# Kernel optimization log

Hardware: AMD Instinct MI355X
Metric: run time of the kernel (lower is better)

## Reference

```python
import jax, jax.numpy as jnp
import numpy as np

N_NODES = 50000
N_EDGES = 800000
IN_DIM = 128
HIDDEN = 64      # out_channels per head (concat=False -> head mean)
HEADS = 2
N_GRAPHS = 64
LN_EPS = 1e-5


def _layer_norm(x, g, b):
    mu = jnp.mean(x, axis=-1, keepdims=True)
    var = jnp.mean((x - mu) ** 2, axis=-1, keepdims=True)
    return (x - mu) * jax.lax.rsqrt(var + LN_EPS) * g + b


def _transformer_conv(x, src, dst, Wq, bq, Wk, bk, Wv, bv, Ws, bs):
    # PyG TransformerConv, concat=False, root_weight=True, beta=False.
    n = x.shape[0]
    q = (x @ Wq + bq).reshape(n, HEADS, -1)[dst]   # [E, H, D] query at target i
    k = (x @ Wk + bk).reshape(n, HEADS, -1)[src]   # [E, H, D] key at source j
    v = (x @ Wv + bv).reshape(n, HEADS, -1)[src]   # [E, H, D] value at source j
    d = q.shape[-1]
    score = jnp.sum(q * k, axis=-1) / jnp.sqrt(jnp.asarray(d, x.dtype))  # [E, H]
    # segment softmax over incoming edges of each target node
    smax = jax.ops.segment_max(score, dst, num_segments=n)
    e = jnp.exp(score - smax[dst])
    denom = jax.ops.segment_sum(e, dst, num_segments=n)
    alpha = e / denom[dst]                                              # [E, H]
    agg = jax.ops.segment_sum(alpha[..., None] * v, dst, num_segments=n)  # [N, H, D]
    out = jnp.mean(agg, axis=1)                     # concat=False -> head mean
    return out + x @ Ws + bs                        # root/skip connection


def setup_inputs() -> dict:
    key = jax.random.key(0)
    ks = jax.random.split(key, 40)
    inp = {}
    inp["x"] = jax.random.normal(ks[0], (N_NODES, IN_DIM), jnp.float32)
    inp["edge_index"] = jax.random.randint(ks[1], (2, N_EDGES), 0, N_NODES, dtype=jnp.int64)
    inp["batch"] = jnp.sort(jax.random.randint(ks[2], (N_NODES,), 0, N_GRAPHS, dtype=jnp.int64))
    dims = [(IN_DIM, HIDDEN), (HIDDEN, HIDDEN), (HIDDEN, HIDDEN)]
    i = 3
    for l, (din, dout) in enumerate(dims):
        for nm in ("q", "k", "v"):
            inp[f"W{nm}{l}"] = jax.random.normal(ks[i], (din, HEADS * dout), jnp.float32) * 0.05; i += 1
            inp[f"b{nm}{l}"] = jnp.zeros((HEADS * dout,), jnp.float32)
        inp[f"Ws{l}"] = jax.random.normal(ks[i], (din, dout), jnp.float32) * 0.05; i += 1
        inp[f"bs{l}"] = jnp.zeros((dout,), jnp.float32)
    for l in range(2):  # LayerNorm after layers 0 and 1 only
        inp[f"g{l}"] = jnp.ones((HIDDEN,), jnp.float32)
        inp[f"beta{l}"] = jnp.zeros((HIDDEN,), jnp.float32)
    inp["Wp"] = jax.random.normal(ks[i], (HIDDEN, 1), jnp.float32) * 0.05
    inp["bp"] = jnp.zeros((1,), jnp.float32)
    return inp


def reference(x, edge_index, batch,
              Wq0, bq0, Wk0, bk0, Wv0, bv0, Ws0, bs0,
              Wq1, bq1, Wk1, bk1, Wv1, bv1, Ws1, bs1,
              Wq2, bq2, Wk2, bk2, Wv2, bv2, Ws2, bs2,
              g0, beta0, g1, beta1, Wp, bp):
    src, dst = edge_index[0], edge_index[1]
    layers = [(Wq0, bq0, Wk0, bk0, Wv0, bv0, Ws0, bs0),
              (Wq1, bq1, Wk1, bk1, Wv1, bv1, Ws1, bs1),
              (Wq2, bq2, Wk2, bk2, Wv2, bv2, Ws2, bs2)]
    lns = [(g0, beta0), (g1, beta1)]
    h = x
    for i, p in enumerate(layers):
        h = _transformer_conv(h, src, dst, *p)
        h = jax.nn.relu(h)  # dropout p=0.0 / eval -> identity
        if i != len(layers) - 1:
            h = _layer_norm(h, *lns[i])
    # global mean pool per graph
    cnt = jax.ops.segment_sum(jnp.ones((h.shape[0],), h.dtype), batch, num_segments=N_GRAPHS)
    pooled = jax.ops.segment_sum(h, batch, num_segments=N_GRAPHS) / jnp.maximum(cnt, 1.0)[:, None]
    return pooled @ Wp + bp
```

## Files before the change

kernel.cpp:

```cpp
#include <hip/hip_runtime.h>
#include <hip/hip_fp16.h>
#include <math.h>

#define HIDDEN 64
#define HEADS 2
#define NCOLS 448
#define KV_COLS 256
#define KV_ROW_BYTES 512
#define N_GRAPHS 64
#define LN_EPS 1e-5f
#define Q_SCALE 0.18033688011112042f

typedef _Float16 half8 __attribute__((ext_vector_type(8)));
typedef float    f32x4 __attribute__((ext_vector_type(4)));


__global__ void cast_f2h_kernel(const float* __restrict__ in, _Float16* __restrict__ out, int n4)
{
    int i = blockIdx.x * 256 + threadIdx.x;
    if (i < n4) {
        float4 v = *(const float4*)&in[i * 4];
        __half2 a = __floats2half2_rn(v.x, v.y);
        __half2 b = __floats2half2_rn(v.z, v.w);
        uint2 pk;
        pk.x = *(unsigned int*)&a;
        pk.y = *(unsigned int*)&b;
        *(uint2*)&out[i * 4] = pk;
    }
}

__global__ void pack_kernel(const float* __restrict__ Wq, const float* __restrict__ Wk,
                            const float* __restrict__ Wv, const float* __restrict__ Ws,
                            const float* __restrict__ bq, const float* __restrict__ bk,
                            const float* __restrict__ bv, const float* __restrict__ bs,
                            _Float16* __restrict__ Bt, float* __restrict__ bcat, int K)
{
    int idx = blockIdx.x * 256 + threadIdx.x;
    int total = NCOLS * K;
    if (idx < total) {
        int c = idx / K, k = idx - c * K;
        float v;
        if      (c < 128) v = Wq[k * 128 + c] * Q_SCALE;
        else if (c < 256) v = Wk[k * 128 + (c - 128)];
        else if (c < 384) v = Wv[k * 128 + (c - 256)];
        else              v = Ws[k * 64  + (c - 384)];
        Bt[idx] = (_Float16)v;
    }
    if (idx < NCOLS) {
        float b;
        if      (idx < 128) b = bq[idx] * Q_SCALE;
        else if (idx < 256) b = bk[idx - 128];
        else if (idx < 384) b = bv[idx - 256];
        else                b = bs[idx - 384];
        bcat[idx] = b;
    }
}

template<int K, int NT>
__device__ __forceinline__ void gemm_body(
    const _Float16* __restrict__ Ah, const float* __restrict__ bias,
    _Float16* __restrict__ qh, float* __restrict__ qsk, __half* __restrict__ kvh,
    const _Float16* Bs, int M, int colBase, int chunkRow0, int tid)
{
    int lane = tid & 63;
    int w    = tid >> 6;
    int fr   = lane & 15;
    int g    = lane >> 4;
    int row0 = chunkRow0 + w * 16;
    int arow = row0 + fr;
    if (arow > M - 1) arow = M - 1;

    f32x4 acc[NT];
    #pragma unroll
    for (int c = 0; c < NT; ++c) acc[c] = (f32x4){0.f, 0.f, 0.f, 0.f};

    #pragma unroll
    for (int ks = 0; ks < K / 32; ++ks) {
        int k0 = ks * 32 + g * 8;
        half8 af = *(const half8*)&Ah[(size_t)arow * K + k0];
        #pragma unroll
        for (int c = 0; c < NT; ++c) {
            int rl   = c * 16 + fr;
            int byte = rl * (K * 2) + k0 * 2;
            int sw   = byte ^ ((rl & 7) << 4);
            half8 bf = *(const half8*)((const char*)Bs + sw);
            acc[c] = __builtin_amdgcn_mfma_f32_16x16x32_f16(af, bf, acc[c], 0, 0, 0);
        }
    }

    #pragma unroll
    for (int c = 0; c < NT; ++c) {
        int col = colBase + c * 16 + fr;
        float bs = bias[col];
        #pragma unroll
        for (int j = 0; j < 4; ++j) {
            int row = row0 + g * 4 + j;
            if (row >= M) continue;
            float o = acc[c][j] + bs;
            if (col < 128) {
                qh[(size_t)row * 128 + col] = (_Float16)o;
            } else if (col >= 384) {
                qsk[(size_t)row * 64 + (col - 384)] = o;
            } else {
                int cc  = col - 128;
                int mat = cc >> 7;
                int hh  = (cc >> 6) & 1;
                int d   = cc & 63;
                int pos = mat * 128 + (d >> 2) * 8 + hh * 4 + (d & 3);
                kvh[(size_t)row * KV_COLS + pos] = __float2half_rn(o);
            }
        }
    }
}

template<int K>
__global__ __launch_bounds__(512, 4) void gemm_mfma_kernel(
    const _Float16* __restrict__ Ah,
    const _Float16* __restrict__ Bt,
    const float* __restrict__ bias,
    _Float16* __restrict__ qh, float* __restrict__ qsk,
    __half* __restrict__ kvh, int M)
{
    __shared__ _Float16 Bs[256 * K];

    int tid    = threadIdx.x;
    int colblk = blockIdx.x & 1;
    int chunk  = blockIdx.x >> 1;
    int colBase = colblk ? 256 : 0;
    int cols    = colblk ? 192 : 256;

    int bytes = cols * K * 2;
    const char* src = (const char*)Bt + (size_t)colBase * K * 2;
    for (int i = tid * 16; i < bytes; i += 512 * 16) {
        int rl = i / (K * 2);
        int sw = i ^ ((rl & 7) << 4);
        *(half8*)((char*)Bs + sw) = *(const half8*)(src + i);
    }
    __syncthreads();

    if (colblk == 0)
        gemm_body<K, 16>(Ah, bias, qh, qsk, kvh, Bs, M, 0,   chunk * 128, tid);
    else
        gemm_body<K, 12>(Ah, bias, qh, qsk, kvh, Bs, M, 256, chunk * 128, tid);
}

__global__ void hist_kernel(const int* __restrict__ dst, int* __restrict__ counts, int E)
{
    int i = blockIdx.x * 256 + threadIdx.x;
    if (i < E) atomicAdd(&counts[dst[i]], 1);
}

__global__ __launch_bounds__(256) void block_reduce_kernel(
    const int* __restrict__ counts, int* __restrict__ bsum, int N)
{
    __shared__ int s[256];
    int t = threadIdx.x;
    int i = blockIdx.x * 256 + t;
    s[t] = (i < N) ? counts[i] : 0;
    __syncthreads();
    #pragma unroll
    for (int o = 128; o; o >>= 1) {
        if (t < o) s[t] += s[t + o];
        __syncthreads();
    }
    if (t == 0) bsum[blockIdx.x] = s[0];
}

__global__ __launch_bounds__(256) void scan_partials_kernel(
    const int* __restrict__ bsum, int* __restrict__ boff, int nb, int* __restrict__ rowN)
{
    __shared__ int s[256];
    int t = threadIdx.x;
    int v = (t < nb) ? bsum[t] : 0;
    s[t] = v;
    __syncthreads();
    #pragma unroll
    for (int o = 1; o < 256; o <<= 1) {
        int x = (t >= o) ? s[t - o] : 0;
        __syncthreads();
        s[t] += x;
        __syncthreads();
    }
    if (t < nb) boff[t] = s[t] - v;
    if (t == nb - 1) rowN[0] = s[t];
}

__global__ __launch_bounds__(256) void block_scan_kernel(
    const int* __restrict__ counts, const int* __restrict__ boff,
    int* __restrict__ row_ptr, int* __restrict__ cursor, int N)
{
    __shared__ int s[256];
    int t = threadIdx.x;
    int i = blockIdx.x * 256 + t;
    int v = (i < N) ? counts[i] : 0;
    s[t] = v;
    __syncthreads();
    #pragma unroll
    for (int o = 1; o < 256; o <<= 1) {
        int x = (t >= o) ? s[t - o] : 0;
        __syncthreads();
        s[t] += x;
        __syncthreads();
    }
    if (i < N) {
        int excl = s[t] - v + boff[blockIdx.x];
        row_ptr[i] = excl;
        cursor[i]  = excl;
    }
}

__global__ void scatter_kernel(const int* __restrict__ ei, int* __restrict__ cursor,
                               int* __restrict__ src_off, int E)
{
    int i = blockIdx.x * 256 + threadIdx.x;
    if (i < E) {
        int d = ei[E + i];
        int pos = atomicAdd(&cursor[d], 1);
        src_off[pos] = ei[i] * KV_ROW_BYTES;
    }
}

__device__ __forceinline__ float dpp_sum16(float x)
{
    float t;
    t = __int_as_float(__builtin_amdgcn_mov_dpp(__float_as_int(x), 0xB1,  0xF, 0xF, true)); x += t;
    t = __int_as_float(__builtin_amdgcn_mov_dpp(__float_as_int(x), 0x4E,  0xF, 0xF, true)); x += t;
    t = __int_as_float(__builtin_amdgcn_mov_dpp(__float_as_int(x), 0x141, 0xF, 0xF, true)); x += t;
    t = __int_as_float(__builtin_amdgcn_mov_dpp(__float_as_int(x), 0x140, 0xF, 0xF, true)); x += t;
    return x;
}

__device__ __forceinline__ void edge_step(
    const uint4& kraw, const uint4& vraw,
    const float4& q0, const float4& q1,
    float& m0, float& s0, float4& a0,
    float& m1, float& s1, float4& a1)
{
    const __half2* kp = (const __half2*)&kraw;
    float2 ka = __half22float2(kp[0]), kb = __half22float2(kp[1]);
    float2 kc = __half22float2(kp[2]), kd = __half22float2(kp[3]);

    float p0 = fmaf(q0.w, kb.y, fmaf(q0.z, kb.x, fmaf(q0.y, ka.y, q0.x * ka.x)));
    float p1 = fmaf(q1.w, kd.y, fmaf(q1.z, kd.x, fmaf(q1.y, kc.y, q1.x * kc.x)));
    float sc0 = dpp_sum16(p0);
    float sc1 = dpp_sum16(p1);

    const __half2* vp = (const __half2*)&vraw;
    float2 va = __half22float2(vp[0]), vb = __half22float2(vp[1]);
    float2 vc = __half22float2(vp[2]), vd = __half22float2(vp[3]);

    float nm0 = fmaxf(m0, sc0);
    float f0  = exp2f(m0 - nm0);
    float w0  = exp2f(sc0 - nm0);
    s0 = fmaf(s0, f0, w0);
    a0.x = fmaf(a0.x, f0, w0 * va.x);
    a0.y = fmaf(a0.y, f0, w0 * va.y);
    a0.z = fmaf(a0.z, f0, w0 * vb.x);
    a0.w = fmaf(a0.w, f0, w0 * vb.y);
    m0 = nm0;

    float nm1 = fmaxf(m1, sc1);
    float f1  = exp2f(m1 - nm1);
    float w1  = exp2f(sc1 - nm1);
    s1 = fmaf(s1, f1, w1);
    a1.x = fmaf(a1.x, f1, w1 * vc.x);
    a1.y = fmaf(a1.y, f1, w1 * vc.y);
    a1.z = fmaf(a1.z, f1, w1 * vd.x);
    a1.w = fmaf(a1.w, f1, w1 * vd.y);
    m1 = nm1;
}

__global__ __launch_bounds__(256) void edge_conv_kernel(
    const _Float16* __restrict__ qh, const float* __restrict__ qsk,
    const __half* __restrict__ kvh,
    const int* __restrict__ row_ptr, const int* __restrict__ src_off,
    const float* __restrict__ gamma, const float* __restrict__ beta,
    float* __restrict__ hout, _Float16* __restrict__ hh, int N, int do_ln)
{
    int wave = threadIdx.x >> 6;
    int lane = threadIdx.x & 63;
    int g    = lane >> 4;
    int sub  = lane & 15;
    int node = blockIdx.x * 4 + wave;
    if (node >= N) return;

    const __half* qrow = (const __half*)(qh + (size_t)node * 128);
    float4 q0, q1;
    {
        uint2 p0 = *(const uint2*)&qrow[sub * 4];
        uint2 p1 = *(const uint2*)&qrow[64 + sub * 4];
        const __half2* h0 = (const __half2*)&p0;
        const __half2* h1 = (const __half2*)&p1;
        float2 a = __half22float2(h0[0]), b = __half22float2(h0[1]);
        float2 c = __half22float2(h1[0]), d = __half22float2(h1[1]);
        q0 = make_float4(a.x, a.y, b.x, b.y);
        q1 = make_float4(c.x, c.y, d.x, d.y);
    }

    int e0 = row_ptr[node], e1 = row_ptr[node + 1];
    int deg = e1 - e0;

    float  m0 = -1e30f, m1 = -1e30f;
    float  s0 = 0.f, s1 = 0.f;
    float4 a0 = make_float4(0.f, 0.f, 0.f, 0.f);
    float4 a1 = make_float4(0.f, 0.f, 0.f, 0.f);

    const char* kvb = (const char*)kvh;
    int  e    = e0 + g;
    bool have = (e < e1);
    uint4 kA, vA, kB, vB;
    if (have) {
        const char* jb = kvb + (size_t)(unsigned)src_off[e];
        kA = *(const uint4*)(jb + sub * 16);
        vA = *(const uint4*)(jb + 256 + sub * 16);
    }

    while (have) {
        int  eB    = e + 4;
        bool haveB = (eB < e1);
        if (haveB) {
            const char* jb = kvb + (size_t)(unsigned)src_off[eB];
            kB = *(const uint4*)(jb + sub * 16);
            vB = *(const uint4*)(jb + 256 + sub * 16);
        }
        edge_step(kA, vA, q0, q1, m0, s0, a0, m1, s1, a1);
        if (!haveB) break;

        int  eA    = eB + 4;
        bool haveA = (eA < e1);
        if (haveA) {
            const char* jb = kvb + (size_t)(unsigned)src_off[eA];
            kA = *(const uint4*)(jb + sub * 16);
            vA = *(const uint4*)(jb + 256 + sub * 16);
        }
        edge_step(kB, vB, q0, q1, m0, s0, a0, m1, s1, a1);

        e = eA; have = haveA;
    }

    #pragma unroll
    for (int offm = 16; offm <= 32; offm <<= 1) {
        float mo0 = __shfl_xor(m0, offm);
        float so0 = __shfl_xor(s0, offm);
        float4 ao0;
        ao0.x = __shfl_xor(a0.x, offm); ao0.y = __shfl_xor(a0.y, offm);
        ao0.z = __shfl_xor(a0.z, offm); ao0.w = __shfl_xor(a0.w, offm);
        float nm = fmaxf(m0, mo0);
        float fa = exp2f(m0 - nm), fb = exp2f(mo0 - nm);
        s0 = s0 * fa + so0 * fb;
        a0.x = a0.x * fa + ao0.x * fb; a0.y = a0.y * fa + ao0.y * fb;
        a0.z = a0.z * fa + ao0.z * fb; a0.w = a0.w * fa + ao0.w * fb;
        m0 = nm;

        float mo1 = __shfl_xor(m1, offm);
        float so1 = __shfl_xor(s1, offm);
        float4 ao1;
        ao1.x = __shfl_xor(a1.x, offm); ao1.y = __shfl_xor(a1.y, offm);
        ao1.z = __shfl_xor(a1.z, offm); ao1.w = __shfl_xor(a1.w, offm);
        nm = fmaxf(m1, mo1);
        fa = exp2f(m1 - nm); fb = exp2f(mo1 - nm);
        s1 = s1 * fa + so1 * fb;
        a1.x = a1.x * fa + ao1.x * fb; a1.y = a1.y * fa + ao1.y * fb;
        a1.z = a1.z * fa + ao1.z * fb; a1.w = a1.w * fa + ao1.w * fb;
        m1 = nm;
    }

    float4 skip = *(const float4*)&qsk[(size_t)node * 64 + sub * 4];
    float4 o;
    if (deg > 0) {
        float r0 = 0.5f / s0, r1 = 0.5f / s1;
        o.x = a0.x * r0 + a1.x * r1 + skip.x;
        o.y = a0.y * r0 + a1.y * r1 + skip.y;
        o.z = a0.z * r0 + a1.z * r1 + skip.z;
        o.w = a0.w * r0 + a1.w * r1 + skip.w;
    } else {
        o = skip;
    }
    o.x = fmaxf(o.x, 0.f); o.y = fmaxf(o.y, 0.f);
    o.z = fmaxf(o.z, 0.f); o.w = fmaxf(o.w, 0.f);

    if (do_ln) {
        float mu = dpp_sum16(o.x + o.y + o.z + o.w) * (1.0f / 64.0f);
        float dx = o.x - mu, dy = o.y - mu, dz = o.z - mu, dw = o.w - mu;
        float var = dpp_sum16(dx * dx + dy * dy + dz * dz + dw * dw) * (1.0f / 64.0f);
        float rs = rsqrtf(var + LN_EPS);
        float4 gm = *(const float4*)&gamma[sub * 4];
        float4 bt = *(const float4*)&beta[sub * 4];
        o.x = dx * rs * gm.x + bt.x;
        o.y = dy * rs * gm.y + bt.y;
        o.z = dz * rs * gm.z + bt.z;
        o.w = dw * rs * gm.w + bt.w;
    }
    if (g == 0) {
        *(float4*)&hout[(size_t)node * HIDDEN + sub * 4] = o;
        __half2 h01 = __floats2half2_rn(o.x, o.y);
        __half2 h23 = __floats2half2_rn(o.z, o.w);
        uint2 pk;
        pk.x = *(unsigned int*)&h01;
        pk.y = *(unsigned int*)&h23;
        *(uint2*)&hh[(size_t)node * HIDDEN + sub * 4] = pk;
    }
}

#define POOL_CHUNK 32
__global__ __launch_bounds__(64) void pool_kernel(const float* __restrict__ h,
                                                  const int* __restrict__ batch,
                                                  float* __restrict__ pooled,
                                                  float* __restrict__ cnt, int N)
{
    int lane = threadIdx.x;
    int start = blockIdx.x * POOL_CHUNK;
    if (start >= N) return;
    int end = min(start + POOL_CHUNK, N);
    int b0 = batch[start];
    int b1 = batch[end - 1];

    if (b0 == b1) {
        float acc = 0.f;
        #pragma unroll 4
        for (int i = start; i < end; ++i)
            acc += h[(size_t)i * HIDDEN + lane];
        atomicAdd(&pooled[b0 * HIDDEN + lane], acc);
        if (lane == 0) atomicAdd(&cnt[b0], (float)(end - start));
    } else {
        float acc = 0.f;
        int cur = b0, c = 0;
        for (int i = start; i < end; ++i) {
            int b = batch[i];
            if (b != cur) {
                atomicAdd(&pooled[cur * HIDDEN + lane], acc);
                if (lane == 0) atomicAdd(&cnt[cur], (float)c);
                acc = 0.f; c = 0; cur = b;
            }
            acc += h[(size_t)i * HIDDEN + lane];
            ++c;
        }
        atomicAdd(&pooled[cur * HIDDEN + lane], acc);
        if (lane == 0) atomicAdd(&cnt[cur], (float)c);
    }
}

__global__ void final_kernel(const float* __restrict__ pooled, const float* __restrict__ cnt,
                             const float* __restrict__ Wp, const float* __restrict__ bp,
                             float* __restrict__ out)
{
    int g = threadIdx.x;
    float c = fmaxf(cnt[g], 1.0f);
    float s = 0.f;
    for (int d = 0; d < HIDDEN; ++d) s += pooled[g * HIDDEN + d] * Wp[d];
    out[g] = s / c + bp[0];
}

extern "C" void kernel_launch(void* const* d_in, const int* in_sizes, int n_in,
                              void* d_out, int out_size, void* d_ws, size_t ws_size,
                              hipStream_t stream)
{
    const float* x    = (const float*)d_in[0];
    const int*   ei   = (const int*)d_in[1];
    const int*   batch= (const int*)d_in[2];

    const float* Wl[3][4];
    const float* bl[3][4];
    for (int l = 0; l < 3; ++l) {
        int b = 3 + l * 8;
        Wl[l][0] = (const float*)d_in[b + 0]; bl[l][0] = (const float*)d_in[b + 1];
        Wl[l][1] = (const float*)d_in[b + 2]; bl[l][1] = (const float*)d_in[b + 3];
        Wl[l][2] = (const float*)d_in[b + 4]; bl[l][2] = (const float*)d_in[b + 5];
        Wl[l][3] = (const float*)d_in[b + 6]; bl[l][3] = (const float*)d_in[b + 7];
    }
    const float* g0    = (const float*)d_in[27];
    const float* beta0 = (const float*)d_in[28];
    const float* g1    = (const float*)d_in[29];
    const float* beta1 = (const float*)d_in[30];
    const float* Wp    = (const float*)d_in[31];
    const float* bp    = (const float*)d_in[32];

    const int N = in_sizes[0] / 128;
    const int E = in_sizes[1] / 2;

    size_t off = 0;
    auto carve = [&](size_t bytes) -> char* {
        char* p = (char*)d_ws + off;
        off = (off + bytes + 255) & ~(size_t)255;
        return p;
    };
    _Float16*  qh     = (_Float16*)carve((size_t)N * 128 * 2);
    float*     qsk    = (float*)carve((size_t)N * 64 * 4);
    __half*    kvh    = (__half*)carve((size_t)N * KV_COLS * 2);
    float*     h      = (float*)carve((size_t)N * HIDDEN * 4);
    _Float16*  hh     = (_Float16*)carve((size_t)N * HIDDEN * 2);
    _Float16*  xh     = (_Float16*)carve((size_t)N * 128 * 2);
    _Float16*  Bt     = (_Float16*)carve((size_t)NCOLS * 128 * 2);
    float*     bcat   = (float*)carve(NCOLS * 4);
    int*       counts = (int*)carve((size_t)N * 4);
    int*       row_ptr= (int*)carve((size_t)(N + 1) * 4);
    int*       cursor = (int*)carve((size_t)N * 4);
    int*       src_off = (int*)carve((size_t)E * 4);
    int*       bsum   = (int*)carve(1024 * 4);
    int*       boff   = (int*)carve(1024 * 4);
    float*     pooled = (float*)carve((size_t)(N_GRAPHS * HIDDEN + N_GRAPHS) * 4);
    float*     cntf   = pooled + N_GRAPHS * HIDDEN;

    const int nb = (N + 255) / 256;

    hipMemsetAsync(counts, 0, (size_t)N * 4, stream);
    hist_kernel<<<(E + 255) / 256, 256, 0, stream>>>(ei + E, counts, E);
    block_reduce_kernel<<<nb, 256, 0, stream>>>(counts, bsum, N);
    scan_partials_kernel<<<1, 256, 0, stream>>>(bsum, boff, nb, &row_ptr[N]);
    block_scan_kernel<<<nb, 256, 0, stream>>>(counts, boff, row_ptr, cursor, N);
    scatter_kernel<<<(E + 255) / 256, 256, 0, stream>>>(ei, cursor, src_off, E);

    {
        int n4 = (N * 128) / 4;
        cast_f2h_kernel<<<(n4 + 255) / 256, 256, 0, stream>>>(x, xh, n4);
    }

    const int gemm_grid = 2 * ((N + 127) / 128);

    for (int l = 0; l < 3; ++l) {
        int K = (l == 0) ? 128 : 64;
        int packTot = NCOLS * K;
        pack_kernel<<<(packTot + 255) / 256, 256, 0, stream>>>(
            Wl[l][0], Wl[l][1], Wl[l][2], Wl[l][3],
            bl[l][0], bl[l][1], bl[l][2], bl[l][3], Bt, bcat, K);
        if (l == 0)
            gemm_mfma_kernel<128><<<gemm_grid, 512, 0, stream>>>(xh, Bt, bcat, qh, qsk, kvh, N);
        else
            gemm_mfma_kernel<64><<<gemm_grid, 512, 0, stream>>>(hh, Bt, bcat, qh, qsk, kvh, N);
        int do_ln = (l < 2) ? 1 : 0;
        const float* gg = (l == 0) ? g0 : g1;
        const float* bb = (l == 0) ? beta0 : beta1;
        edge_conv_kernel<<<(N + 3) / 4, 256, 0, stream>>>(
            qh, qsk, kvh, row_ptr, src_off, gg, bb, h, hh, N, do_ln);
    }

    hipMemsetAsync(pooled, 0, (size_t)(N_GRAPHS * HIDDEN + N_GRAPHS) * 4, stream);
    pool_kernel<<<(N + POOL_CHUNK - 1) / POOL_CHUNK, 64, 0, stream>>>(h, batch, pooled, cntf, N);
    final_kernel<<<1, 64, 0, stream>>>(pooled, cntf, Wp, bp, (float*)d_out);
}
```

Before: 409.2 us.

## Pack all layer weights in one launch and split GEMM into four column blocks

The three per-layer weight-packing launches become a single kernel that writes separate packed buffers and biases for each layer, and it runs before the layer loop. The MFMA GEMM now splits the 448 output columns into four 112-column blocks instead of 256/192 halves. This shrinks shared memory and accumulator registers per block, raises the occupancy hint from 4 to 6, and doubles the grid. In exchange the A tile is re-read four times instead of twice, and the 112-column blocks may not line up with the q/k/v/skip boundaries inside gemm_body.

After: 399.4 us. 2.4% less time.

```diff
diff --git a/kernel.cpp b/kernel.cpp
--- a/kernel.cpp
+++ b/kernel.cpp
@@ -29,30 +29,65 @@
     }
 }
 
-__global__ void pack_kernel(const float* __restrict__ Wq, const float* __restrict__ Wk,
-                            const float* __restrict__ Wv, const float* __restrict__ Ws,
-                            const float* __restrict__ bq, const float* __restrict__ bk,
-                            const float* __restrict__ bv, const float* __restrict__ bs,
-                            _Float16* __restrict__ Bt, float* __restrict__ bcat, int K)
+__device__ __forceinline__ float pack_elem(
+    int c, int k, int K,
+    const float* Wq, const float* Wk, const float* Wv, const float* Ws)
+{
+    if      (c < 128) return Wq[k * 128 + c] * Q_SCALE;
+    else if (c < 256) return Wk[k * 128 + (c - 128)];
+    else if (c < 384) return Wv[k * 128 + (c - 256)];
+    else              return Ws[k * 64  + (c - 384)];
+}
+
+__device__ __forceinline__ float pack_bias(
+    int c, const float* bq, const float* bk, const float* bv, const float* bs)
+{
+    if      (c < 128) return bq[c] * Q_SCALE;
+    else if (c < 256) return bk[c - 128];
+    else if (c < 384) return bv[c - 256];
+    else              return bs[c - 384];
+}
+
+#define L0_SZ (448 * 128)
+#define L12_SZ (448 * 64)
+#define PACK_TOTAL (L0_SZ + 2 * L12_SZ + 3 * NCOLS)
+
+__global__ void pack3_kernel(
+    const float* __restrict__ Wq0, const float* __restrict__ Wk0,
+    const float* __restrict__ Wv0, const float* __restrict__ Ws0,
+    const float* __restrict__ bq0, const float* __restrict__ bk0,
+    const float* __restrict__ bv0, const float* __restrict__ bs0,
+    const float* __restrict__ Wq1, const float* __restrict__ Wk1,
+    const float* __restrict__ Wv1, const float* __restrict__ Ws1,
+    const float* __restrict__ bq1, const float* __restrict__ bk1,
+    const float* __restrict__ bv1, const float* __restrict__ bs1,
+    const float* __restrict__ Wq2, const float* __restrict__ Wk2,
+    const float* __restrict__ Wv2, const float* __restrict__ Ws2,
+    const float* __restrict__ bq2, const float* __restrict__ bk2,
+    const float* __restrict__ bv2, const float* __restrict__ bs2,
+    _Float16* __restrict__ Bt0, _Float16* __restrict__ Bt1,
+    _Float16* __restrict__ Bt2, float* __restrict__ bc)
 {
     int idx = blockIdx.x * 256 + threadIdx.x;
-    int total = NCOLS * K;
-    if (idx < total) {
-        int c = idx / K, k = idx - c * K;
-        float v;
-        if      (c < 128) v = Wq[k * 128 + c] * Q_SCALE;
-        else if (c < 256) v = Wk[k * 128 + (c - 128)];
-        else if (c < 384) v = Wv[k * 128 + (c - 256)];
-        else              v = Ws[k * 64  + (c - 384)];
-        Bt[idx] = (_Float16)v;
-    }
-    if (idx < NCOLS) {
+    if (idx < L0_SZ) {
+        int c = idx / 128, k = idx - c * 128;
+        Bt0[idx] = (_Float16)pack_elem(c, k, 128, Wq0, Wk0, Wv0, Ws0);
+    } else if (idx < L0_SZ + L12_SZ) {
+        int i = idx - L0_SZ;
+        int c = i / 64, k = i - c * 64;
+        Bt1[i] = (_Float16)pack_elem(c, k, 64, Wq1, Wk1, Wv1, Ws1);
+    } else if (idx < L0_SZ + 2 * L12_SZ) {
+        int i = idx - L0_SZ - L12_SZ;
+        int c = i / 64, k = i - c * 64;
+        Bt2[i] = (_Float16)pack_elem(c, k, 64, Wq2, Wk2, Wv2, Ws2);
+    } else if (idx < PACK_TOTAL) {
+        int i = idx - L0_SZ - 2 * L12_SZ;
+        int l = i / NCOLS, c = i - l * NCOLS;
         float b;
-        if      (idx < 128) b = bq[idx] * Q_SCALE;
-        else if (idx < 256) b = bk[idx - 128];
-        else if (idx < 384) b = bv[idx - 256];
-        else                b = bs[idx - 384];
-        bcat[idx] = b;
+        if      (l == 0) b = pack_bias(c, bq0, bk0, bv0, bs0);
+        else if (l == 1) b = pack_bias(c, bq1, bk1, bv1, bs1);
+        else             b = pack_bias(c, bq2, bk2, bv2, bs2);
+        bc[l * NCOLS + c] = b;
     }
 }
 
@@ -114,22 +149,21 @@
 }
 
 template<int K>
-__global__ __launch_bounds__(512, 4) void gemm_mfma_kernel(
+__global__ __launch_bounds__(512, 6) void gemm_mfma_kernel(
     const _Float16* __restrict__ Ah,
     const _Float16* __restrict__ Bt,
     const float* __restrict__ bias,
     _Float16* __restrict__ qh, float* __restrict__ qsk,
     __half* __restrict__ kvh, int M)
 {
-    __shared__ _Float16 Bs[256 * K];
-
-    int tid    = threadIdx.x;
-    int colblk = blockIdx.x & 1;
-    int chunk  = blockIdx.x >> 1;
-    int colBase = colblk ? 256 : 0;
-    int cols    = colblk ? 192 : 256;
-
-    int bytes = cols * K * 2;
+    __shared__ _Float16 Bs[112 * K];
+
+    int tid     = threadIdx.x;
+    int colblk  = blockIdx.x & 3;
+    int chunk   = blockIdx.x >> 2;
+    int colBase = colblk * 112;
+
+    int bytes = 112 * K * 2;
     const char* src = (const char*)Bt + (size_t)colBase * K * 2;
     for (int i = tid * 16; i < bytes; i += 512 * 16) {
         int rl = i / (K * 2);
@@ -138,10 +172,7 @@
     }
     __syncthreads();
 
-    if (colblk == 0)
-        gemm_body<K, 16>(Ah, bias, qh, qsk, kvh, Bs, M, 0,   chunk * 128, tid);
-    else
-        gemm_body<K, 12>(Ah, bias, qh, qsk, kvh, Bs, M, 256, chunk * 128, tid);
+    gemm_body<K, 7>(Ah, bias, qh, qsk, kvh, Bs, M, colBase, chunk * 128, tid);
 }
 
 __global__ void hist_kernel(const int* __restrict__ dst, int* __restrict__ counts, int E)
@@ -490,8 +521,10 @@
     float*     h      = (float*)carve((size_t)N * HIDDEN * 4);
     _Float16*  hh     = (_Float16*)carve((size_t)N * HIDDEN * 2);
     _Float16*  xh     = (_Float16*)carve((size_t)N * 128 * 2);
-    _Float16*  Bt     = (_Float16*)carve((size_t)NCOLS * 128 * 2);
-    float*     bcat   = (float*)carve(NCOLS * 4);
+    _Float16*  Bt0    = (_Float16*)carve((size_t)L0_SZ * 2);
+    _Float16*  Bt1    = (_Float16*)carve((size_t)L12_SZ * 2);
+    _Float16*  Bt2    = (_Float16*)carve((size_t)L12_SZ * 2);
+    float*     bc     = (float*)carve(3 * NCOLS * 4);
     int*       counts = (int*)carve((size_t)N * 4);
     int*       row_ptr= (int*)carve((size_t)(N + 1) * 4);
     int*       cursor = (int*)carve((size_t)N * 4);
@@ -510,23 +543,28 @@
     block_scan_kernel<<<nb, 256, 0, stream>>>(counts, boff, row_ptr, cursor, N);
     scatter_kernel<<<(E + 255) / 256, 256, 0, stream>>>(ei, cursor, src_off, E);
 
+    pack3_kernel<<<(PACK_TOTAL + 255) / 256, 256, 0, stream>>>(
+        Wl[0][0], Wl[0][1], Wl[0][2], Wl[0][3], bl[0][0], bl[0][1], bl[0][2], bl[0][3],
+        Wl[1][0], Wl[1][1], Wl[1][2], Wl[1][3], bl[1][0], bl[1][1], bl[1][2], bl[1][3],
+        Wl[2][0], Wl[2][1], Wl[2][2], Wl[2][3], bl[2][0], bl[2][1], bl[2][2], bl[2][3],
+        Bt0, Bt1, Bt2, bc);
     {
         int n4 = (N * 128) / 4;
         cast_f2h_kernel<<<(n4 + 255) / 256, 256, 0, stream>>>(x, xh, n4);
     }
 
-    const int gemm_grid = 2 * ((N + 127) / 128);
+    const int gemm_grid = 4 * ((N + 127) / 128);
 
     for (int l = 0; l < 3; ++l) {
-        int K = (l == 0) ? 128 : 64;
-        int packTot = NCOLS * K;
-        pack_kernel<<<(packTot + 255) / 256, 256, 0, stream>>>(
-            Wl[l][0], Wl[l][1], Wl[l][2], Wl[l][3],
-            bl[l][0], bl[l][1], bl[l][2], bl[l][3], Bt, bcat, K);
         if (l == 0)
-            gemm_mfma_kernel<128><<<gemm_grid, 512, 0, stream>>>(xh, Bt, bcat, qh, qsk, kvh, N);
+            gemm_mfma_kernel<128><<<gemm_grid, 512, 0, stream>>>(
+                xh, Bt0, bc, qh, qsk, kvh, N);
+        else if (l == 1)
+            gemm_mfma_kernel<64><<<gemm_grid, 512, 0, stream>>>(
+                hh, Bt1, bc + NCOLS, qh, qsk, kvh, N);
         else
-            gemm_mfma_kernel<64><<<gemm_grid, 512, 0, stream>>>(hh, Bt, bcat, qh, qsk, kvh, N);
+            gemm_mfma_kernel<64><<<gemm_grid, 512, 0, stream>>>(
+                hh, Bt2, bc + 2 * NCOLS, qh, qsk, kvh, N);
         int do_ln = (l < 2) ? 1 : 0;
         const float* gg = (l == 0) ? g0 : g1;
         const float* bb = (l == 0) ? beta0 : beta1;
```
